# Performance work log

Hardware: AMD Instinct MI355X
Metric: run time of the kernel (lower is better)

The kernel has to match this reference:

```python
import jax, jax.numpy as jnp
import numpy as np

# Dims: batch, in-ch, out-ch, deform kernel, channels-per-offset-group, input H/W
B, CIN, COUT, K, CPG, H, W = 16, 64, 64, 3, 8, 130, 130
G = CIN // CPG                 # number of deformable offset groups = 8
HO, WO = H - 2, W - 2          # conv1 (3x3, VALID) output == deform-conv output (3x3, VALID)
DN = ('NCHW', 'OIHW', 'NCHW')


def _conv(x, w, b):
    y = jax.lax.conv_general_dilated(x, w, (1, 1), 'VALID', dimension_numbers=DN)
    return y + b[None, :, None, None]


def setup_inputs() -> dict:
    key = jax.random.key(0)
    k0, k1, k2, k3 = jax.random.split(key, 4)
    def wn(k, shape, fan_in, scale=1.0):
        return jax.random.normal(k, shape, jnp.float32) * (scale / np.sqrt(fan_in))
    return {
        'x':  jax.random.normal(k0, (B, CIN, H, W), jnp.float32),
        'w1': wn(k1, (CIN, CIN, 3, 3), CIN * 9),
        'b1': jnp.zeros((CIN,), jnp.float32),
        # small scale so predicted offsets stay in a realistic sub-pixel/pixel range
        'w2': wn(k2, (G * 2 * K * K, CIN, 1, 1), CIN, scale=0.1),
        'b2': jnp.zeros((G * 2 * K * K,), jnp.float32),
        'wd': wn(k3, (COUT, CIN, K, K), CIN * K * K),
    }


def _deform_conv(x, off, wd):
    # x: [B,CIN,H,W], off: [B,G*2*K*K,HO,WO], wd: [COUT,CIN,K,K]
    Bq, Cin, Hx, Wx = x.shape
    offr = off.reshape(Bq, G, K, K, 2, HO, WO)     # (dy, dx) per group/kernel-pos/pixel
    xg = x.reshape(Bq, G, CPG, Hx * Wx)            # grouped input, flat spatial
    hh = jnp.arange(HO, dtype=x.dtype)[:, None]
    ww = jnp.arange(WO, dtype=x.dtype)[None, :]
    out = jnp.zeros((Bq, COUT, HO, WO), x.dtype)

    def gather(yi, xi, valid):
        # yi/xi: clipped int coords [B,G,HO,WO]; valid: 0/1 mask (zero padding outside)
        idx = (yi * Wx + xi).reshape(Bq, G, 1, HO * WO)
        v = jnp.take_along_axis(xg, jnp.broadcast_to(idx, (Bq, G, CPG, HO * WO)), axis=-1)
        return v.reshape(Bq, G, CPG, HO, WO) * valid[:, :, None, :, :]

    for i in range(K):
        for j in range(K):
            py = offr[:, :, i, j, 0] + (hh + i)    # [B,G,HO,WO] sample row (float)
            px = offr[:, :, i, j, 1] + (ww + j)    # [B,G,HO,WO] sample col (float)
            y0 = jnp.floor(py); x0 = jnp.floor(px)
            ly = py - y0;       lx = px - x0
            y0i = y0.astype(jnp.int32); x0i = x0.astype(jnp.int32)
            y1i = y0i + 1;              x1i = x0i + 1
            inb = lambda yi, xi: ((yi >= 0) & (yi < Hx) & (xi >= 0) & (xi < Wx)).astype(x.dtype)
            yc0 = jnp.clip(y0i, 0, Hx - 1); yc1 = jnp.clip(y1i, 0, Hx - 1)
            xc0 = jnp.clip(x0i, 0, Wx - 1); xc1 = jnp.clip(x1i, 0, Wx - 1)
            v = (((1 - ly) * (1 - lx))[:, :, None] * gather(yc0, xc0, inb(y0i, x0i))
               + ((1 - ly) * lx)[:, :, None]       * gather(yc0, xc1, inb(y0i, x1i))
               + (ly * (1 - lx))[:, :, None]       * gather(yc1, xc0, inb(y1i, x0i))
               + (ly * lx)[:, :, None]             * gather(yc1, xc1, inb(y1i, x1i)))
            # accumulate this kernel tap: v [B,G,CPG,HO,WO] x wd[:,:,i,j] [COUT,G,CPG]
            out = out + jnp.einsum('bgchw,ogc->bohw', v, wd[:, :, i, j].reshape(COUT, G, CPG))
    return out


def reference(x, w1, b1, w2, b2, wd):
    off = _conv(_conv(x, w1, b1), w2, b2)          # [B, G*2*K*K, HO, WO]
    y = _deform_conv(x, off, wd)                   # [B, COUT, HO, WO]
    return (y, off)
```

## Files before the change

### kernel.cpp

```cpp
#include <hip/hip_runtime.h>

typedef unsigned short u16;
typedef unsigned int u32;
typedef __attribute__((ext_vector_type(8))) short bfrag;
typedef __attribute__((ext_vector_type(4))) float ffrag;

constexpr int B_ = 16, CIN = 64, COUT = 64, G = 8, CPG = 8;
constexpr int H = 130, W = 130, HO = 128, WO = 128;
constexpr int OFFC = 144;
constexpr int PLANE_IN = H * W;
constexpr int PLANE_OUT = HO * WO;

constexpr size_t WB1_BYTE = 36864 * 4;
constexpr size_t WB2_BYTE = WB1_BYTE + 36864 * 2;
constexpr size_t XT_BYTE  = 262144;
constexpr size_t XT_SIZE  = (size_t)B_ * PLANE_IN * 64 * 2;

__device__ __forceinline__ u16 f2bf(float f) {
    union { u32 u; float f; } t; t.f = f;
    return (u16)((t.u + 0x7FFFu + ((t.u >> 16) & 1u)) >> 16);
}
__device__ __forceinline__ float bf2f(short h) {
    union { u32 u; float f; } t; t.u = ((u32)(u16)h) << 16;
    return t.f;
}

__global__ void prep_weights(const float* __restrict__ w1,
                             const float* __restrict__ wd,
                             const float* __restrict__ w2,
                             float* __restrict__ wsf) {
    u16* wdB = (u16*)wsf;
    u16* wB1 = (u16*)((char*)wsf + WB1_BYTE);
    u16* wB2 = (u16*)((char*)wsf + WB2_BYTE);
    int idx = blockIdx.x * 256 + threadIdx.x;
    if (idx < 36864) {
        int co = idx / 576, r = idx % 576;
        int t = r >> 6, ci = r & 63;
        wdB[idx] = f2bf(wd[(co * 64 + ci) * 9 + t]);
    } else if (idx < 73728) {
        int j = idx - 36864;
        int co = j / 576, r = j % 576;
        int t = r >> 6, ci = r & 63;
        wB1[j] = f2bf(w1[(co * 64 + ci) * 9 + t]);
    } else if (idx < 82944) {
        int j = idx - 73728;
        wB2[j] = f2bf(w2[j]);
    }
}

__global__ __launch_bounds__(256) void x_to_nhwc(const float* __restrict__ x,
                                                 u16* __restrict__ xt) {
    int p = blockIdx.x * 256 + threadIdx.x;
    if (p >= B_ * PLANE_IN) return;
    int b = p / PLANE_IN, pp = p % PLANE_IN;
    const float* xb = x + (size_t)b * CIN * PLANE_IN + pp;
    u16* dst = xt + (size_t)p * 64;
    #pragma unroll
    for (int oct = 0; oct < 8; ++oct) {
        union { u16 h[8]; uint4 q; } pk;
        #pragma unroll
        for (int j = 0; j < 8; ++j)
            pk.h[j] = f2bf(xb[(size_t)(oct * 8 + j) * PLANE_IN]);
        *(uint4*)(dst + oct * 8) = pk.q;
    }
}

union ConvSmem {
    u16 xs[324 * 72];
    u16 hs[4][64][72];
};

template<bool XT>
__global__ __launch_bounds__(256) void conv12(const float* __restrict__ x,
                                              const u16* __restrict__ xt,
                                              const float* __restrict__ b1,
                                              const float* __restrict__ b2,
                                              const float* __restrict__ wsf,
                                              float* __restrict__ off_out) {
    __shared__ ConvSmem sm;
    const u16* wB1 = (const u16*)((const char*)wsf + WB1_BYTE);
    const u16* wB2 = (const u16*)((const char*)wsf + WB2_BYTE);
    const int b = blockIdx.z;
    const int y0 = blockIdx.y * 16, x0 = blockIdx.x * 16;
    const int tid = threadIdx.x;
    const int wave = tid >> 6, lane = tid & 63;
    const int n16 = lane & 15, quad = lane >> 4;

    if constexpr (XT) {
        const u16* xtb = xt + (size_t)b * PLANE_IN * 64;
        for (int idx = tid; idx < 324 * 8; idx += 256) {
            int p = idx >> 3, oct = idx & 7;
            *(bfrag*)&sm.xs[p * 72 + oct * 8] =
                *(const bfrag*)&xtb[((size_t)(y0 + p / 18) * W + x0 + p % 18) * 64 + oct * 8];
        }
    } else {
        const float* xb = x + (size_t)b * CIN * PLANE_IN;
        for (int idx = tid; idx < 324 * 64; idx += 256) {
            int ci = idx / 324, p = idx % 324;
            float v = xb[(size_t)ci * PLANE_IN + (y0 + p / 18) * W + (x0 + p % 18)];
            sm.xs[p * 72 + ci] = f2bf(v);
        }
    }
    __syncthreads();

    ffrag acc[4][4];
    #pragma unroll
    for (int nt = 0; nt < 4; ++nt) {
        float bv = b1[nt * 16 + n16];
        #pragma unroll
        for (int mt = 0; mt < 4; ++mt) acc[mt][nt] = ffrag{bv, bv, bv, bv};
    }

    #pragma unroll
    for (int s = 0; s < 18; ++s) {
        const int tap = s >> 1, cib = (s & 1) * 32;
        const int ti = tap / 3, tj = tap % 3;
        bfrag a[4], bb[4];
        #pragma unroll
        for (int mt = 0; mt < 4; ++mt) {
            int p = (wave * 4 + mt + ti) * 18 + n16 + tj;
            a[mt] = *(const bfrag*)&sm.xs[p * 72 + cib + quad * 8];
        }
        #pragma unroll
        for (int nt = 0; nt < 4; ++nt)
            bb[nt] = *(const bfrag*)&wB1[(nt * 16 + n16) * 576 + tap * 64 + cib + quad * 8];
        #pragma unroll
        for (int mt = 0; mt < 4; ++mt)
            #pragma unroll
            for (int nt = 0; nt < 4; ++nt)
                acc[mt][nt] = __builtin_amdgcn_mfma_f32_16x16x32_bf16(
                    a[mt], bb[nt], acc[mt][nt], 0, 0, 0);
    }

    __syncthreads();

    #pragma unroll
    for (int mt = 0; mt < 4; ++mt)
        #pragma unroll
        for (int nt = 0; nt < 4; ++nt)
            #pragma unroll
            for (int r = 0; r < 4; ++r)
                sm.hs[wave][mt * 16 + quad * 4 + r][nt * 16 + n16] = f2bf(acc[mt][nt][r]);
    __syncthreads();

    bfrag a2[4][2];
    #pragma unroll
    for (int mt = 0; mt < 4; ++mt)
        #pragma unroll
        for (int s2 = 0; s2 < 2; ++s2)
            a2[mt][s2] = *(const bfrag*)&sm.hs[wave][mt * 16 + n16][s2 * 32 + quad * 8];

    float* offb = off_out + (size_t)b * OFFC * PLANE_OUT;
    #pragma unroll 1
    for (int nt2 = 0; nt2 < 9; ++nt2) {
        bfrag b2f[2];
        #pragma unroll
        for (int s2 = 0; s2 < 2; ++s2)
            b2f[s2] = *(const bfrag*)&wB2[(nt2 * 16 + n16) * 64 + s2 * 32 + quad * 8];
        float bv = b2[nt2 * 16 + n16];
        #pragma unroll
        for (int mt = 0; mt < 4; ++mt) {
            ffrag acc2 = ffrag{bv, bv, bv, bv};
            acc2 = __builtin_amdgcn_mfma_f32_16x16x32_bf16(a2[mt][0], b2f[0], acc2, 0, 0, 0);
            acc2 = __builtin_amdgcn_mfma_f32_16x16x32_bf16(a2[mt][1], b2f[1], acc2, 0, 0, 0);
            float* dst = offb + (size_t)(nt2 * 16 + n16) * PLANE_OUT
                       + (y0 + wave * 4 + mt) * WO + x0 + quad * 4;
            *(ffrag*)dst = acc2;
        }
    }
}

template<bool XT>
__global__ __launch_bounds__(512, 4) void deform_k(const float* __restrict__ x,
                                                   const u16* __restrict__ xt,
                                                   const float* __restrict__ wsf,
                                                   const float* __restrict__ off_in,
                                                   float* __restrict__ y_out) {
    const u16* wdB = (const u16*)wsf;

    const int wg = blockIdx.x;
    const int swz = (wg & 7) * 128 + (wg >> 3);
    const int b = swz >> 6, sp = swz & 63;
    const int y0 = (sp >> 3) * 16, x0 = (sp & 7) * 16;

    const int tid = threadIdx.x;
    const int wave = tid >> 6, lane = tid & 63;
    const int n16 = lane & 15, quad = lane >> 4;
    const int wo = x0 + n16;

    const float* offbase = off_in + (size_t)b * OFFC * PLANE_OUT + x0 + n16;
    const u16* xtb = xt + (size_t)b * PLANE_IN * 64;
    const float* xb = x + (size_t)b * CIN * PLANE_IN;

    ffrag acc[2][4];
    #pragma unroll
    for (int mt = 0; mt < 2; ++mt)
        #pragma unroll
        for (int nt = 0; nt < 4; ++nt) acc[mt][nt] = ffrag{0.f, 0.f, 0.f, 0.f};

    #pragma unroll 1
    for (int t = 0; t < 9; ++t) {
        const int ki = t / 3, kj = t % 3;
        bfrag a0[2], a1[2];

        #pragma unroll
        for (int mt = 0; mt < 2; ++mt) {
            const int ho = y0 + wave * 2 + mt;
            #pragma unroll
            for (int half = 0; half < 2; ++half) {
                const int g = quad + half * 4;
                const float* ob = offbase + ho * WO + (size_t)((g * 9 + t) * 2) * PLANE_OUT;
                float dy = ob[0];
                float dx = ob[PLANE_OUT];
                float py = dy + (float)(ho + ki);
                float px = dx + (float)(wo + kj);
                float y0f = floorf(py), x0f = floorf(px);
                float ly = py - y0f, lx = px - x0f;
                int yi0 = (int)y0f, xi0 = (int)x0f;
                int yi1 = yi0 + 1, xi1 = xi0 + 1;
                float vy0 = (yi0 >= 0 && yi0 < H) ? 1.f : 0.f;
                float vy1 = (yi1 >= 0 && yi1 < H) ? 1.f : 0.f;
                float vx0 = (xi0 >= 0 && xi0 < W) ? 1.f : 0.f;
                float vx1 = (xi1 >= 0 && xi1 < W) ? 1.f : 0.f;
                float w00 = (1.f - ly) * (1.f - lx) * vy0 * vx0;
                float w01 = (1.f - ly) * lx         * vy0 * vx1;
                float w10 = ly * (1.f - lx)         * vy1 * vx0;
                float w11 = ly * lx                 * vy1 * vx1;
                int yc0 = min(max(yi0, 0), H - 1), yc1 = min(max(yi1, 0), H - 1);
                int xc0 = min(max(xi0, 0), W - 1), xc1 = min(max(xi1, 0), W - 1);
                union { u16 h[8]; bfrag f; } pk;
                if constexpr (XT) {
                    bfrag q00 = *(const bfrag*)&xtb[((size_t)(yc0 * W + xc0)) * 64 + g * 8];
                    bfrag q01 = *(const bfrag*)&xtb[((size_t)(yc0 * W + xc1)) * 64 + g * 8];
                    bfrag q10 = *(const bfrag*)&xtb[((size_t)(yc1 * W + xc0)) * 64 + g * 8];
                    bfrag q11 = *(const bfrag*)&xtb[((size_t)(yc1 * W + xc1)) * 64 + g * 8];
                    #pragma unroll
                    for (int j = 0; j < 8; ++j) {
                        float v = w00 * bf2f(q00[j]) + w01 * bf2f(q01[j])
                                + w10 * bf2f(q10[j]) + w11 * bf2f(q11[j]);
                        pk.h[j] = f2bf(v);
                    }
                } else {
                    int i00 = yc0 * W + xc0, i01 = yc0 * W + xc1;
                    int i10 = yc1 * W + xc0, i11 = yc1 * W + xc1;
                    const float* xg = xb + (size_t)g * CPG * PLANE_IN;
                    #pragma unroll
                    for (int cc = 0; cc < 8; ++cc) {
                        const float* xp = xg + cc * PLANE_IN;
                        float v = w00 * xp[i00] + w01 * xp[i01]
                                + w10 * xp[i10] + w11 * xp[i11];
                        pk.h[cc] = f2bf(v);
                    }
                }
                if (half == 0) a0[mt] = pk.f; else a1[mt] = pk.f;
            }
        }

        #pragma unroll
        for (int nt = 0; nt < 4; ++nt) {
            const u16* wp = &wdB[(size_t)(nt * 16 + n16) * 576 + t * 64 + quad * 8];
            bfrag b0 = *(const bfrag*)wp;
            bfrag b1 = *(const bfrag*)(wp + 32);
            #pragma unroll
            for (int mt = 0; mt < 2; ++mt) {
                acc[mt][nt] = __builtin_amdgcn_mfma_f32_16x16x32_bf16(a0[mt], b0, acc[mt][nt], 0, 0, 0);
                acc[mt][nt] = __builtin_amdgcn_mfma_f32_16x16x32_bf16(a1[mt], b1, acc[mt][nt], 0, 0, 0);
            }
        }
    }

    float* yb = y_out + (size_t)b * COUT * PLANE_OUT;
    #pragma unroll
    for (int nt = 0; nt < 4; ++nt)
        #pragma unroll
        for (int mt = 0; mt < 2; ++mt) {
            float* dst = yb + (size_t)(nt * 16 + n16) * PLANE_OUT
                       + (y0 + wave * 2 + mt) * WO + x0 + quad * 4;
            *(ffrag*)dst = acc[mt][nt];
        }
}

extern "C" void kernel_launch(void* const* d_in, const int* in_sizes, int n_in,
                              void* d_out, int out_size, void* d_ws, size_t ws_size,
                              hipStream_t stream) {
    const float* x  = (const float*)d_in[0];
    const float* w1 = (const float*)d_in[1];
    const float* b1 = (const float*)d_in[2];
    const float* w2 = (const float*)d_in[3];
    const float* b2 = (const float*)d_in[4];
    const float* wd = (const float*)d_in[5];
    float* y_out = (float*)d_out;
    float* off_out = y_out + (size_t)B_ * COUT * PLANE_OUT;
    float* wsf = (float*)d_ws;
    u16* xt = (u16*)((char*)d_ws + XT_BYTE);
    const bool use_xt = ws_size >= XT_BYTE + XT_SIZE;

    prep_weights<<<324, 256, 0, stream>>>(w1, wd, w2, wsf);
    if (use_xt) {
        x_to_nhwc<<<(B_ * PLANE_IN + 255) / 256, 256, 0, stream>>>(x, xt);
        conv12<true><<<dim3(8, 8, B_), 256, 0, stream>>>(x, xt, b1, b2, wsf, off_out);
        deform_k<true><<<1024, 512, 0, stream>>>(x, xt, wsf, off_out, y_out);
    } else {
        conv12<false><<<dim3(8, 8, B_), 256, 0, stream>>>(x, xt, b1, b2, wsf, off_out);
        deform_k<false><<<1024, 512, 0, stream>>>(x, xt, wsf, off_out, y_out);
    }
}
```

Before: 537.9 us.

## Swizzle conv LDS layout and software-pipeline deform gathers with smaller blocks

The conv12 shared-memory tiles switch from padded 72-element rows to 128-byte rows with an XOR swizzle, to avoid LDS bank conflicts without padding. The deform kernel now uses 256-thread blocks covering 8 output rows and launches twice as many blocks. It prefetches the next tap's offsets one iteration ahead and interleaves the bilinear corner loads, weight loads and interpolation math to hide gather latency. The extra live registers for prefetched values may lower occupancy.

Result: no change. 530.2 us (-1.4%).

```diff
diff --git a/kernel.cpp b/kernel.cpp
--- a/kernel.cpp
+++ b/kernel.cpp
@@ -66,9 +66,12 @@
 }
 
 union ConvSmem {
-    u16 xs[324 * 72];
-    u16 hs[4][64][72];
+    char xsb[324 * 128];
+    char hsb[4][64 * 128];
 };
+__device__ __forceinline__ int swz128(int row, int bytecol) {
+    return row * 128 + (bytecol ^ ((row & 7) << 4));
+}
 
 template<bool XT>
 __global__ __launch_bounds__(256) void conv12(const float* __restrict__ x,
@@ -90,7 +93,7 @@
         const u16* xtb = xt + (size_t)b * PLANE_IN * 64;
         for (int idx = tid; idx < 324 * 8; idx += 256) {
             int p = idx >> 3, oct = idx & 7;
-            *(bfrag*)&sm.xs[p * 72 + oct * 8] =
+            *(bfrag*)(sm.xsb + swz128(p, oct * 16)) =
                 *(const bfrag*)&xtb[((size_t)(y0 + p / 18) * W + x0 + p % 18) * 64 + oct * 8];
         }
     } else {
@@ -98,7 +101,7 @@
         for (int idx = tid; idx < 324 * 64; idx += 256) {
             int ci = idx / 324, p = idx % 324;
             float v = xb[(size_t)ci * PLANE_IN + (y0 + p / 18) * W + (x0 + p % 18)];
-            sm.xs[p * 72 + ci] = f2bf(v);
+            *(u16*)(sm.xsb + swz128(p, ci * 2)) = f2bf(v);
         }
     }
     __syncthreads();
@@ -119,7 +122,7 @@
         #pragma unroll
         for (int mt = 0; mt < 4; ++mt) {
             int p = (wave * 4 + mt + ti) * 18 + n16 + tj;
-            a[mt] = *(const bfrag*)&sm.xs[p * 72 + cib + quad * 8];
+            a[mt] = *(const bfrag*)(sm.xsb + swz128(p, cib * 2 + quad * 16));
         }
         #pragma unroll
         for (int nt = 0; nt < 4; ++nt)
@@ -140,7 +143,8 @@
         for (int nt = 0; nt < 4; ++nt)
             #pragma unroll
             for (int r = 0; r < 4; ++r)
-                sm.hs[wave][mt * 16 + quad * 4 + r][nt * 16 + n16] = f2bf(acc[mt][nt][r]);
+                *(u16*)(sm.hsb[wave] + swz128(mt * 16 + quad * 4 + r, (nt * 16 + n16) * 2))
+                    = f2bf(acc[mt][nt][r]);
     __syncthreads();
 
     bfrag a2[4][2];
@@ -148,7 +152,8 @@
     for (int mt = 0; mt < 4; ++mt)
         #pragma unroll
         for (int s2 = 0; s2 < 2; ++s2)
-            a2[mt][s2] = *(const bfrag*)&sm.hs[wave][mt * 16 + n16][s2 * 32 + quad * 8];
+            a2[mt][s2] = *(const bfrag*)(sm.hsb[wave]
+                        + swz128(mt * 16 + n16, s2 * 64 + quad * 16));
 
     float* offb = off_out + (size_t)b * OFFC * PLANE_OUT;
     #pragma unroll 1
@@ -170,8 +175,19 @@
     }
 }
 
+__device__ __forceinline__ bfrag interp4(const bfrag* q, const float* w) {
+    union { u16 h[8]; bfrag f; } pk;
+    #pragma unroll
+    for (int j = 0; j < 8; ++j) {
+        float v = w[0] * bf2f(q[0][j]) + w[1] * bf2f(q[1][j])
+                + w[2] * bf2f(q[2][j]) + w[3] * bf2f(q[3][j]);
+        pk.h[j] = f2bf(v);
+    }
+    return pk.f;
+}
+
 template<bool XT>
-__global__ __launch_bounds__(512, 4) void deform_k(const float* __restrict__ x,
+__global__ __launch_bounds__(256, 2) void deform_k(const float* __restrict__ x,
                                                    const u16* __restrict__ xt,
                                                    const float* __restrict__ wsf,
                                                    const float* __restrict__ off_in,
@@ -179,9 +195,9 @@
     const u16* wdB = (const u16*)wsf;
 
     const int wg = blockIdx.x;
-    const int swz = (wg & 7) * 128 + (wg >> 3);
-    const int b = swz >> 6, sp = swz & 63;
-    const int y0 = (sp >> 3) * 16, x0 = (sp & 7) * 16;
+    const int swz = (wg & 7) * 256 + (wg >> 3);
+    const int b = swz >> 7, sp = swz & 127;
+    const int y0 = (sp >> 3) * 8, x0 = (sp & 7) * 16;
 
     const int tid = threadIdx.x;
     const int wave = tid >> 6, lane = tid & 63;
@@ -198,73 +214,126 @@
         #pragma unroll
         for (int nt = 0; nt < 4; ++nt) acc[mt][nt] = ffrag{0.f, 0.f, 0.f, 0.f};
 
+    float pdy[4], pdx[4];
+    #pragma unroll
+    for (int tk = 0; tk < 4; ++tk) {
+        const int mt = tk >> 1, g = quad + (tk & 1) * 4;
+        const float* ob = offbase + (y0 + wave * 2 + mt) * WO
+                        + (size_t)(g * 9 * 2) * PLANE_OUT;
+        pdy[tk] = ob[0];
+        pdx[tk] = ob[PLANE_OUT];
+    }
+
     #pragma unroll 1
     for (int t = 0; t < 9; ++t) {
         const int ki = t / 3, kj = t % 3;
-        bfrag a0[2], a1[2];
-
-        #pragma unroll
-        for (int mt = 0; mt < 2; ++mt) {
+
+        float dyv[4], dxv[4];
+        #pragma unroll
+        for (int tk = 0; tk < 4; ++tk) { dyv[tk] = pdy[tk]; dxv[tk] = pdx[tk]; }
+
+        if (t < 8) {
+            #pragma unroll
+            for (int tk = 0; tk < 4; ++tk) {
+                const int mt = tk >> 1, g = quad + (tk & 1) * 4;
+                const float* ob = offbase + (y0 + wave * 2 + mt) * WO
+                                + (size_t)((g * 9 + t + 1) * 2) * PLANE_OUT;
+                pdy[tk] = ob[0];
+                pdx[tk] = ob[PLANE_OUT];
+            }
+        }
+
+        int idxq[4][4];
+        float wq[4][4];
+        #pragma unroll
+        for (int tk = 0; tk < 4; ++tk) {
+            const int mt = tk >> 1, g = quad + (tk & 1) * 4;
             const int ho = y0 + wave * 2 + mt;
-            #pragma unroll
-            for (int half = 0; half < 2; ++half) {
-                const int g = quad + half * 4;
-                const float* ob = offbase + ho * WO + (size_t)((g * 9 + t) * 2) * PLANE_OUT;
-                float dy = ob[0];
-                float dx = ob[PLANE_OUT];
-                float py = dy + (float)(ho + ki);
-                float px = dx + (float)(wo + kj);
-                float y0f = floorf(py), x0f = floorf(px);
-                float ly = py - y0f, lx = px - x0f;
-                int yi0 = (int)y0f, xi0 = (int)x0f;
-                int yi1 = yi0 + 1, xi1 = xi0 + 1;
-                float vy0 = (yi0 >= 0 && yi0 < H) ? 1.f : 0.f;
-                float vy1 = (yi1 >= 0 && yi1 < H) ? 1.f : 0.f;
-                float vx0 = (xi0 >= 0 && xi0 < W) ? 1.f : 0.f;
-                float vx1 = (xi1 >= 0 && xi1 < W) ? 1.f : 0.f;
-                float w00 = (1.f - ly) * (1.f - lx) * vy0 * vx0;
-                float w01 = (1.f - ly) * lx         * vy0 * vx1;
-                float w10 = ly * (1.f - lx)         * vy1 * vx0;
-                float w11 = ly * lx                 * vy1 * vx1;
-                int yc0 = min(max(yi0, 0), H - 1), yc1 = min(max(yi1, 0), H - 1);
-                int xc0 = min(max(xi0, 0), W - 1), xc1 = min(max(xi1, 0), W - 1);
+            float py = dyv[tk] + (float)(ho + ki);
+            float px = dxv[tk] + (float)(wo + kj);
+            float y0f = floorf(py), x0f = floorf(px);
+            float ly = py - y0f, lx = px - x0f;
+            int yi0 = (int)y0f, xi0 = (int)x0f;
+            int yi1 = yi0 + 1, xi1 = xi0 + 1;
+            float vy0 = (yi0 >= 0 && yi0 < H) ? 1.f : 0.f;
+            float vy1 = (yi1 >= 0 && yi1 < H) ? 1.f : 0.f;
+            float vx0 = (xi0 >= 0 && xi0 < W) ? 1.f : 0.f;
+            float vx1 = (xi1 >= 0 && xi1 < W) ? 1.f : 0.f;
+            wq[tk][0] = (1.f - ly) * (1.f - lx) * vy0 * vx0;
+            wq[tk][1] = (1.f - ly) * lx         * vy0 * vx1;
+            wq[tk][2] = ly * (1.f - lx)         * vy1 * vx0;
+            wq[tk][3] = ly * lx                 * vy1 * vx1;
+            int yc0 = min(max(yi0, 0), H - 1), yc1 = min(max(yi1, 0), H - 1);
+            int xc0 = min(max(xi0, 0), W - 1), xc1 = min(max(xi1, 0), W - 1);
+            idxq[tk][0] = (yc0 * W + xc0) * 64 + g * 8;
+            idxq[tk][1] = (yc0 * W + xc1) * 64 + g * 8;
+            idxq[tk][2] = (yc1 * W + xc0) * 64 + g * 8;
+            idxq[tk][3] = (yc1 * W + xc1) * 64 + g * 8;
+        }
+
+        bfrag frag[4];
+        if constexpr (XT) {
+            bfrag q0[4], q1[4], q2[4], q3[4];
+            #pragma unroll
+            for (int c = 0; c < 4; ++c) q0[c] = *(const bfrag*)&xtb[idxq[0][c]];
+            #pragma unroll
+            for (int c = 0; c < 4; ++c) q1[c] = *(const bfrag*)&xtb[idxq[1][c]];
+            bfrag bw0[4], bw1[4];
+            #pragma unroll
+            for (int nt = 0; nt < 4; ++nt) {
+                const u16* wp = &wdB[(size_t)(nt * 16 + n16) * 576 + t * 64 + quad * 8];
+                bw0[nt] = *(const bfrag*)wp;
+                bw1[nt] = *(const bfrag*)(wp + 32);
+            }
+            frag[0] = interp4(q0, wq[0]);
+            #pragma unroll
+            for (int c = 0; c < 4; ++c) q2[c] = *(const bfrag*)&xtb[idxq[2][c]];
+            frag[1] = interp4(q1, wq[1]);
+            #pragma unroll
+            for (int c = 0; c < 4; ++c) q3[c] = *(const bfrag*)&xtb[idxq[3][c]];
+            frag[2] = interp4(q2, wq[2]);
+            frag[3] = interp4(q3, wq[3]);
+
+            #pragma unroll
+            for (int nt = 0; nt < 4; ++nt)
+                #pragma unroll
+                for (int mt = 0; mt < 2; ++mt) {
+                    acc[mt][nt] = __builtin_amdgcn_mfma_f32_16x16x32_bf16(
+                        frag[mt * 2 + 0], bw0[nt], acc[mt][nt], 0, 0, 0);
+                    acc[mt][nt] = __builtin_amdgcn_mfma_f32_16x16x32_bf16(
+                        frag[mt * 2 + 1], bw1[nt], acc[mt][nt], 0, 0, 0);
+                }
+        } else {
+            #pragma unroll
+            for (int tk = 0; tk < 4; ++tk) {
+                const int g = quad + (tk & 1) * 4;
+                const float* xg = xb + (size_t)g * CPG * PLANE_IN;
                 union { u16 h[8]; bfrag f; } pk;
-                if constexpr (XT) {
-                    bfrag q00 = *(const bfrag*)&xtb[((size_t)(yc0 * W + xc0)) * 64 + g * 8];
-                    bfrag q01 = *(const bfrag*)&xtb[((size_t)(yc0 * W + xc1)) * 64 + g * 8];
-                    bfrag q10 = *(const bfrag*)&xtb[((size_t)(yc1 * W + xc0)) * 64 + g * 8];
-                    bfrag q11 = *(const bfrag*)&xtb[((size_t)(yc1 * W + xc1)) * 64 + g * 8];
-                    #pragma unroll
-                    for (int j = 0; j < 8; ++j) {
-                        float v = w00 * bf2f(q00[j]) + w01 * bf2f(q01[j])
-                                + w10 * bf2f(q10[j]) + w11 * bf2f(q11[j]);
-                        pk.h[j] = f2bf(v);
-                    }
-                } else {
-                    int i00 = yc0 * W + xc0, i01 = yc0 * W + xc1;
-                    int i10 = yc1 * W + xc0, i11 = yc1 * W + xc1;
-                    const float* xg = xb + (size_t)g * CPG * PLANE_IN;
-                    #pragma unroll
-                    for (int cc = 0; cc < 8; ++cc) {
-                        const float* xp = xg + cc * PLANE_IN;
-                        float v = w00 * xp[i00] + w01 * xp[i01]
-                                + w10 * xp[i10] + w11 * xp[i11];
-                        pk.h[cc] = f2bf(v);
-                    }
+                #pragma unroll
+                for (int cc = 0; cc < 8; ++cc) {
+                    const float* xp = xg + cc * PLANE_IN;
+                    int sh = (idxq[tk][0] - g * 8) / 64;
+                    int s01 = (idxq[tk][1] - g * 8) / 64;
+                    int s10 = (idxq[tk][2] - g * 8) / 64;
+                    int s11 = (idxq[tk][3] - g * 8) / 64;
+                    float v = wq[tk][0] * xp[sh] + wq[tk][1] * xp[s01]
+                            + wq[tk][2] * xp[s10] + wq[tk][3] * xp[s11];
+                    pk.h[cc] = f2bf(v);
                 }
-                if (half == 0) a0[mt] = pk.f; else a1[mt] = pk.f;
+                frag[tk] = pk.f;
             }
-        }
-
-        #pragma unroll
-        for (int nt = 0; nt < 4; ++nt) {
-            const u16* wp = &wdB[(size_t)(nt * 16 + n16) * 576 + t * 64 + quad * 8];
-            bfrag b0 = *(const bfrag*)wp;
-            bfrag b1 = *(const bfrag*)(wp + 32);
-            #pragma unroll
-            for (int mt = 0; mt < 2; ++mt) {
-                acc[mt][nt] = __builtin_amdgcn_mfma_f32_16x16x32_bf16(a0[mt], b0, acc[mt][nt], 0, 0, 0);
-                acc[mt][nt] = __builtin_amdgcn_mfma_f32_16x16x32_bf16(a1[mt], b1, acc[mt][nt], 0, 0, 0);
+            #pragma unroll
+            for (int nt = 0; nt < 4; ++nt) {
+                const u16* wp = &wdB[(size_t)(nt * 16 + n16) * 576 + t * 64 + quad * 8];
+                bfrag b0 = *(const bfrag*)wp;
+                bfrag b1 = *(const bfrag*)(wp + 32);
+                #pragma unroll
+                for (int mt = 0; mt < 2; ++mt) {
+                    acc[mt][nt] = __builtin_amdgcn_mfma_f32_16x16x32_bf16(
+                        frag[mt * 2 + 0], b0, acc[mt][nt], 0, 0, 0);
+                    acc[mt][nt] = __builtin_amdgcn_mfma_f32_16x16x32_bf16(
+                        frag[mt * 2 + 1], b1, acc[mt][nt], 0, 0, 0);
+                }
             }
         }
     }
@@ -299,9 +368,9 @@
     if (use_xt) {
         x_to_nhwc<<<(B_ * PLANE_IN + 255) / 256, 256, 0, stream>>>(x, xt);
         conv12<true><<<dim3(8, 8, B_), 256, 0, stream>>>(x, xt, b1, b2, wsf, off_out);
-        deform_k<true><<<1024, 512, 0, stream>>>(x, xt, wsf, off_out, y_out);
+        deform_k<true><<<2048, 256, 0, stream>>>(x, xt, wsf, off_out, y_out);
     } else {
         conv12<false><<<dim3(8, 8, B_), 256, 0, stream>>>(x, xt, b1, b2, wsf, off_out);
-        deform_k<false><<<1024, 512, 0, stream>>>(x, xt, wsf, off_out, y_out);
-    }
-}
+        deform_k<false><<<2048, 256, 0, stream>>>(x, xt, wsf, off_out, y_out);
+    }
+}
```
